# Performance work log

Hardware: AMD Instinct MI355X
Metric: run time of the kernel (lower is better)

## Reference

```python
import jax, jax.numpy as jnp
import numpy as np

B, S, D, H = 2, 2048, 1024, 16
DH = D // H  # dim per head (dim_singl_head)
SCALE = 0.02


def layer_norm(x, g, b, eps=1e-5):
    m = jnp.mean(x, axis=-1, keepdims=True)
    v = jnp.mean((x - m) ** 2, axis=-1, keepdims=True)
    return (x - m) / jnp.sqrt(v + eps) * g + b


def setup_inputs() -> dict:
    key = jax.random.key(0)
    ks = jax.random.split(key, 12)
    return {
        "query": jax.random.normal(ks[0], (B, S, D), jnp.float32),
        "key": jax.random.normal(ks[1], (B, S, D), jnp.float32),
        "value": jax.random.normal(ks[2], (B, S, D), jnp.float32),
        "mask": jax.random.randint(ks[3], (B, S), 0, 2).astype(jnp.int32),
        "Wq": jax.random.normal(ks[4], (D, D), jnp.float32) * SCALE,
        "bq": jnp.zeros((D,), jnp.float32),
        "Wk": jax.random.normal(ks[5], (D, D), jnp.float32) * SCALE,
        "bk": jnp.zeros((D,), jnp.float32),
        "Wv": jax.random.normal(ks[6], (D, D), jnp.float32) * SCALE,
        "bv": jnp.zeros((D,), jnp.float32),
        "g_att": jnp.ones((DH,), jnp.float32),
        "b_att": jnp.zeros((DH,), jnp.float32),
        "Wres": jax.random.normal(ks[7], (D, D), jnp.float32) * SCALE,
        "bres": jnp.zeros((D,), jnp.float32),
        "g_out": jnp.ones((D,), jnp.float32),
        "b_out": jnp.zeros((D,), jnp.float32),
    }


def reference(query, key, value, mask, Wq, bq, Wk, bk, Wv, bv,
              g_att, b_att, Wres, bres, g_out, b_out):
    # split heads: torch's split(dh,-1)+cat(dim=0) == [H,B,S,dh] layout
    def heads(x):
        return x.reshape(B, S, H, DH).transpose(2, 0, 1, 3)  # [H,B,S,dh]

    q = heads(query @ Wq + bq)
    k = heads(key @ Wk + bk)
    v = heads(value @ Wv + bv)

    # additive mask: (1-mask)*-1e9, broadcast [1,B,1,Sk]
    madd = (1.0 - mask.astype(q.dtype))[None, :, None, :] * -1e9

    scores = jnp.einsum('hbqd,hbkd->hbqk', q, k) / np.float32(np.sqrt(DH))
    w = jax.nn.softmax(scores + madd, axis=-1)
    out = jnp.einsum('hbqk,hbkd->hbqd', w, v)

    out = out + q                         # residual_att
    out = layer_norm(out, g_att, b_att)   # per-head LayerNorm on dh

    # concat heads back: [H,B,S,dh] -> [B,S,H*dh]
    out = out.transpose(1, 2, 0, 3).reshape(B, S, D)

    out = out + jnp.tanh(out @ Wres + bres)  # residual_out branch
    out = layer_norm(out, g_out, b_out)      # norm_out
    return jnp.tanh(out)                     # final activation
```

## Files before the change

### kernel.cpp

```cpp
#include <hip/hip_runtime.h>
#include <cstdint>
#include <cstddef>

#define BB 2
#define SS 2048
#define DD 1024
#define HH 16
#define DHH 64
#define MROWS (BB*SS)

typedef short short8 __attribute__((ext_vector_type(8)));
typedef short short4v __attribute__((ext_vector_type(4)));
typedef float floatx4 __attribute__((ext_vector_type(4)));
typedef float floatx16 __attribute__((ext_vector_type(16)));
typedef unsigned int uint4v __attribute__((ext_vector_type(4)));

#define GAS __attribute__((address_space(1)))
#define LAS __attribute__((address_space(3)))

__device__ __forceinline__ float4 ld4(const float* p) { return *(const float4*)p; }

__device__ __forceinline__ short f2bf(float x) {
    unsigned u = __builtin_bit_cast(unsigned, x);
    unsigned r = (u + 0x7fffu + ((u >> 16) & 1u)) >> 16;
    return (short)r;
}

__device__ __forceinline__ unsigned cvtpk(float lo, float hi) {
    unsigned r;
    asm("v_cvt_pk_bf16_f32 %0, %1, %2" : "=v"(r) : "v"(lo), "v"(hi));
    return r;
}

__device__ __forceinline__ void gl_lds16(const short* g, short* l) {
    __builtin_amdgcn_global_load_lds((const GAS unsigned int*)g,
                                     (LAS unsigned int*)l, 16, 0, 0);
}

__global__ __launch_bounds__(256) void convert_kernel(
    const float* __restrict__ s0, const float* __restrict__ s1, const float* __restrict__ s2,
    short* __restrict__ d0, short* __restrict__ d1, short* __restrict__ d2)
{
    const float* s; short* d;
    if (blockIdx.z == 0)      { s = s0; d = d0; }
    else if (blockIdx.z == 1) { s = s1; d = d1; }
    else                      { s = s2; d = d2; }
    size_t idx = ((size_t)blockIdx.x * 256 + threadIdx.x) * 8;
    float4 a = ld4(s + idx);
    float4 b = ld4(s + idx + 4);
    short8 p;
    p[0] = f2bf(a.x); p[1] = f2bf(a.y); p[2] = f2bf(a.z); p[3] = f2bf(a.w);
    p[4] = f2bf(b.x); p[5] = f2bf(b.y); p[6] = f2bf(b.z); p[7] = f2bf(b.w);
    *(short8*)(d + idx) = p;
}

__global__ __launch_bounds__(256) void transpose_w_kernel(
    const float* __restrict__ W0, const float* __restrict__ W1,
    const float* __restrict__ W2, const float* __restrict__ W3,
    short* __restrict__ T0, short* __restrict__ T1,
    short* __restrict__ T2, short* __restrict__ T3)
{
    const float* W; short* T;
    if (blockIdx.z == 0)      { W = W0; T = T0; }
    else if (blockIdx.z == 1) { W = W1; T = T1; }
    else if (blockIdx.z == 2) { W = W2; T = T2; }
    else                      { W = W3; T = T3; }

    __shared__ short tile[64 * 72];
    const int t  = threadIdx.x;
    const int k0 = blockIdx.x * 64, n0 = blockIdx.y * 64;
#pragma unroll
    for (int i = 0; i < 4; i++) {
        int flat = i * 256 + t;
        int row = flat >> 4;
        int c4  = (flat & 15) * 4;
        float4 v = ld4(W + (size_t)(k0 + row) * DD + n0 + c4);
        tile[(c4 + 0) * 72 + row] = f2bf(v.x);
        tile[(c4 + 1) * 72 + row] = f2bf(v.y);
        tile[(c4 + 2) * 72 + row] = f2bf(v.z);
        tile[(c4 + 3) * 72 + row] = f2bf(v.w);
    }
    __syncthreads();
#pragma unroll
    for (int i = 0; i < 4; i++) {
        int flat = i * 256 + t;
        int nrow = flat >> 4;
        int kc   = (flat & 15) * 4;
        short4v pk = *(short4v*)&tile[nrow * 72 + kc];
        *(short4v*)(T + (size_t)(n0 + nrow) * DD + k0 + kc) = pk;
    }
}

__global__ __launch_bounds__(256) void gemm_bf16_kernel(
    const short* __restrict__ A0, const short* __restrict__ A1, const short* __restrict__ A2,
    const short* __restrict__ Bt0, const short* __restrict__ Bt1, const short* __restrict__ Bt2,
    const float* __restrict__ b0, const float* __restrict__ b1, const float* __restrict__ b2,
    float* __restrict__ Cf0, float* __restrict__ Cf1, float* __restrict__ Cf2,
    short* __restrict__ Cb0, short* __restrict__ Cb1, short* __restrict__ Cb2,
    short* __restrict__ Ct0, short* __restrict__ Ct1, short* __restrict__ Ct2,
    float cs0, float cs1, float cs2)
{
    const short* A; const short* Bt; const float* bias;
    float* Cf; short* Cb; short* Ct; float cbs;
    if (blockIdx.z == 0)      { A = A0; Bt = Bt0; bias = b0; Cf = Cf0; Cb = Cb0; Ct = Ct0; cbs = cs0; }
    else if (blockIdx.z == 1) { A = A1; Bt = Bt1; bias = b1; Cf = Cf1; Cb = Cb1; Ct = Ct1; cbs = cs1; }
    else                      { A = A2; Bt = Bt2; bias = b2; Cf = Cf2; Cb = Cb2; Ct = Ct2; cbs = cs2; }

    __shared__ __align__(16) short As[128 * 32];
    __shared__ __align__(16) short Bs[128 * 32];

    const int tid  = threadIdx.x;
    const int lane = tid & 63;
    const int wave = tid >> 6;
    const int quad = lane >> 4;
    const int l15  = lane & 15;
    const int m0 = blockIdx.y * 128;
    const int n0 = blockIdx.x * 128;
    const int wr = (wave >> 1) * 64;
    const int wc = (wave & 1) * 64;

    floatx4 acc[4][4];
#pragma unroll
    for (int mt = 0; mt < 4; mt++)
#pragma unroll
        for (int nt = 0; nt < 4; nt++) acc[mt][nt] = (floatx4)0.0f;

    for (int k0 = 0; k0 < DD; k0 += 32) {
        __syncthreads();
#pragma unroll
        for (int j = 0; j < 2; j++) {
            int chunk = j * 256 + tid;
            int row = chunk >> 2;
            int ch  = chunk & 3;
            gl_lds16(A  + (size_t)(m0 + row) * DD + k0 + ch * 8, &As[chunk * 8]);
            gl_lds16(Bt + (size_t)(n0 + row) * DD + k0 + ch * 8, &Bs[chunk * 8]);
        }
        __syncthreads();

        short8 af[4], bf[4];
#pragma unroll
        for (int mt = 0; mt < 4; mt++)
            af[mt] = *(const short8*)&As[(wr + mt * 16 + l15) * 32 + quad * 8];
#pragma unroll
        for (int nt = 0; nt < 4; nt++)
            bf[nt] = *(const short8*)&Bs[(wc + nt * 16 + l15) * 32 + quad * 8];
#pragma unroll
        for (int mt = 0; mt < 4; mt++)
#pragma unroll
            for (int nt = 0; nt < 4; nt++)
                acc[mt][nt] = __builtin_amdgcn_mfma_f32_16x16x32_bf16(af[mt], bf[nt], acc[mt][nt], 0, 0, 0);
    }

    float biasv[4];
#pragma unroll
    for (int nt = 0; nt < 4; nt++) biasv[nt] = bias[n0 + wc + nt * 16 + l15];

    if (Cf || Cb) {
#pragma unroll
        for (int mt = 0; mt < 4; mt++)
#pragma unroll
            for (int r = 0; r < 4; r++) {
                const int m = m0 + wr + mt * 16 + quad * 4 + r;
                const size_t rowb = (size_t)m * DD + n0 + wc;
#pragma unroll
                for (int nt = 0; nt < 4; nt++) {
                    float v = acc[mt][nt][r] + biasv[nt];
                    if (Cf) Cf[rowb + nt * 16 + l15] = v;
                    if (Cb) Cb[rowb + nt * 16 + l15] = f2bf(v * cbs);
                }
            }
    }
    if (Ct) {
#pragma unroll
        for (int mt = 0; mt < 4; mt++) {
            const int mbase = m0 + wr + mt * 16 + quad * 4;
            const int bb = mbase >> 11;
            const int s0 = mbase & 2047;
#pragma unroll
            for (int nt = 0; nt < 4; nt++) {
                const int c = n0 + wc + nt * 16 + l15;
                short4v pk;
#pragma unroll
                for (int r = 0; r < 4; r++) pk[r] = f2bf(acc[mt][nt][r] + biasv[nt]);
                *(short4v*)(Ct + ((size_t)(bb * 1024 + c)) * SS + s0) = pk;
            }
        }
    }
}

__global__ __launch_bounds__(256) void repack_kernel(
    const short* __restrict__ Kb, const short* __restrict__ Vt,
    const int* __restrict__ mask,
    short* __restrict__ Kf, short* __restrict__ Vf, float* __restrict__ maddf)
{
    const int t = threadIdx.x;
    if (blockIdx.z == 0) {
        const int b = blockIdx.x >> 6, kg = blockIdx.x & 63;
#pragma unroll
        for (int i = 0; i < 16; i++) {
            const int h = i, ks = t >> 6, lane = t & 63;
            const int c = lane & 31, hi = lane >> 5;
            short8 v = *(const short8*)(Kb + (size_t)(b * 2048 + kg * 32 + c) * 1024
                                        + h * 64 + ks * 16 + hi * 8);
            *(short8*)(Kf + ((size_t)((b * 16 + h) * 64 + kg)) * 2048 + ks * 512 + lane * 8) = v;
        }
    } else if (blockIdx.x < 64) {
        const int b = blockIdx.x >> 5, kt = blockIdx.x & 31;
#pragma unroll
        for (int i = 0; i < 32; i++) {
            const int flat = i * 256 + t;
            const int h = flat >> 9, rest = flat & 511;
            const int tp = rest >> 7, dg = (rest >> 6) & 1, lane = rest & 63;
            const int c = lane & 31, hi = lane >> 5;
            short8 v = *(const short8*)(Vt + (size_t)(b * 1024 + h * 64 + dg * 32 + c) * 2048
                                        + kt * 64 + tp * 16 + hi * 8);
            *(short8*)(Vf + ((size_t)((b * 16 + h) * 32 + kt)) * 4096
                       + (tp * 2 + dg) * 512 + lane * 8) = v;
        }
    } else if (blockIdx.x < 66) {
        const int b = blockIdx.x - 64;
#pragma unroll
        for (int j = 0; j < 8; j++) {
            const int idx = t * 8 + j;
            maddf[b * 2048 + idx] = (1.0f - (float)mask[b * 2048 + idx]) * -1e9f;
        }
    }
}

__device__ __forceinline__ void attn_tile(
    const short8 (&kf)[2][4], const short8 (&vf)[8], const short8 (&qf)[4],
    const float* mdb, int kt, floatx16 (&o)[2], float& lsum)
{
#pragma unroll
    for (int g = 0; g < 2; g++) {
        floatx16 acc = (floatx16)0.0f;
        __builtin_amdgcn_s_setprio(1);
#pragma unroll
        for (int ks = 0; ks < 4; ks++)
            acc = __builtin_amdgcn_mfma_f32_32x32x16_bf16(kf[g][ks], qf[ks], acc, 0, 0, 0);
        __builtin_amdgcn_s_setprio(0);
        float p[16];
#pragma unroll
        for (int a = 0; a < 4; a++) {
            float4 mr = *(const float4*)(mdb + kt * 64 + g * 32 + a * 8);
            p[4 * a + 0] = __builtin_exp2f(acc[4 * a + 0] + mr.x);
            p[4 * a + 1] = __builtin_exp2f(acc[4 * a + 1] + mr.y);
            p[4 * a + 2] = __builtin_exp2f(acc[4 * a + 2] + mr.z);
            p[4 * a + 3] = __builtin_exp2f(acc[4 * a + 3] + mr.w);
        }
        lsum += ((p[0] + p[1]) + (p[2] + p[3])) + ((p[4] + p[5]) + (p[6] + p[7]))
              + ((p[8] + p[9]) + (p[10] + p[11])) + ((p[12] + p[13]) + (p[14] + p[15]));
#pragma unroll
        for (int t2 = 0; t2 < 2; t2++) {
            unsigned w0 = cvtpk(p[8 * t2 + 0], p[8 * t2 + 1]);
            unsigned w1 = cvtpk(p[8 * t2 + 2], p[8 * t2 + 3]);
            unsigned w2 = cvtpk(p[8 * t2 + 4], p[8 * t2 + 5]);
            unsigned w3 = cvtpk(p[8 * t2 + 6], p[8 * t2 + 7]);
            asm volatile("v_permlane32_swap_b32 %0, %1" : "+v"(w0), "+v"(w2));
            asm volatile("v_permlane32_swap_b32 %0, %1" : "+v"(w1), "+v"(w3));
            uint4v u = {w0, w1, w2, w3};
            short8 pa = __builtin_bit_cast(short8, u);
            __builtin_amdgcn_s_setprio(1);
#pragma unroll
            for (int dg = 0; dg < 2; dg++)
                o[dg] = __builtin_amdgcn_mfma_f32_32x32x16_bf16(
                    pa, vf[(g * 2 + t2) * 2 + dg], o[dg], 0, 0, 0);
            __builtin_amdgcn_s_setprio(0);
        }
    }
}

__global__ __launch_bounds__(256, 2) void attn_mfma_kernel(
    const short* __restrict__ Qb, const short* __restrict__ Kf, const short* __restrict__ Vf,
    const float* __restrict__ Qf, const float* __restrict__ maddf,
    const float* __restrict__ g_att, const float* __restrict__ b_att,
    float* __restrict__ X, short* __restrict__ Xb)
{
    const int tid  = threadIdx.x;
    const int lane = tid & 63;
    const int wave = tid >> 6;
    const int hi   = lane >> 5;
    const int c    = lane & 31;

    const int h  = blockIdx.y;
    const int b  = blockIdx.z;
    const int q0 = blockIdx.x * 128;
    const int bS = b * SS;

    const short* kfb = Kf + ((size_t)(b * 16 + h) * 64) * 2048 + lane * 8;
    const short* vfb = Vf + ((size_t)(b * 16 + h) * 32) * 4096 + lane * 8;
    const float* mdb = maddf + b * 2048 + hi * 4;

    short8 qf[4];
#pragma unroll
    for (int ks = 0; ks < 4; ks++)
        qf[ks] = *(const short8*)(Qb +
            (size_t)(bS + q0 + wave * 32 + c) * DD + h * 64 + ks * 16 + hi * 8);

    floatx16 o[2];
    o[0] = (floatx16)0.0f;
    o[1] = (floatx16)0.0f;
    float lsum = 0.0f;

    short8 kfA[2][4], kfB[2][4], vf[8];
#pragma unroll
    for (int g = 0; g < 2; g++)
#pragma unroll
        for (int ks = 0; ks < 4; ks++)
            kfA[g][ks] = *(const short8*)(kfb + (size_t)(0 * 2 + g) * 2048 + ks * 512);

    for (int kt = 0; kt < 32; kt += 2) {
#pragma unroll
        for (int j = 0; j < 8; j++)
            vf[j] = *(const short8*)(vfb + (size_t)kt * 4096 + j * 512);
#pragma unroll
        for (int g = 0; g < 2; g++)
#pragma unroll
            for (int ks = 0; ks < 4; ks++)
                kfB[g][ks] = *(const short8*)(kfb + (size_t)((kt + 1) * 2 + g) * 2048 + ks * 512);
        attn_tile(kfA, vf, qf, mdb, kt, o, lsum);

#pragma unroll
        for (int j = 0; j < 8; j++)
            vf[j] = *(const short8*)(vfb + (size_t)(kt + 1) * 4096 + j * 512);
        const int ktn = (kt + 2 < 32) ? (kt + 2) : 31;
#pragma unroll
        for (int g = 0; g < 2; g++)
#pragma unroll
            for (int ks = 0; ks < 4; ks++)
                kfA[g][ks] = *(const short8*)(kfb + (size_t)(ktn * 2 + g) * 2048 + ks * 512);
        attn_tile(kfB, vf, qf, mdb, kt + 1, o, lsum);
    }

    lsum += __shfl_xor(lsum, 32);
    const float rl = 1.0f / lsum;

    const float g0v = g_att[c], g1v = g_att[32 + c];
    const float b0v = b_att[c], b1v = b_att[32 + c];

#pragma unroll
    for (int r = 0; r < 16; r++) {
        const int rloc = (r & 3) + 8 * (r >> 2) + 4 * hi;
        const float rlr = __shfl(rl, rloc);
        const int row = q0 + wave * 32 + rloc;
        const size_t base = (size_t)(bS + row) * DD + h * 64;
        float x0 = o[0][r] * rlr + Qf[base + c];
        float x1 = o[1][r] * rlr + Qf[base + 32 + c];
        float s = x0 + x1;
#pragma unroll
        for (int off = 1; off < 32; off <<= 1) s += __shfl_xor(s, off);
        const float mu = s * (1.0f / 64.0f);
        float d0 = x0 - mu, d1 = x1 - mu;
        float v = d0 * d0 + d1 * d1;
#pragma unroll
        for (int off = 1; off < 32; off <<= 1) v += __shfl_xor(v, off);
        const float rstd = rsqrtf(v * (1.0f / 64.0f) + 1e-5f);
        float y0 = d0 * rstd * g0v + b0v;
        float y1 = d1 * rstd * g1v + b1v;
        X[base + c]      = y0;
        X[base + 32 + c] = y1;
        Xb[base + c]      = f2bf(y0);
        Xb[base + 32 + c] = f2bf(y1);
    }
}

__global__ __launch_bounds__(256) void lnout_kernel(
    const float* __restrict__ X, const float* __restrict__ Y,
    const float* __restrict__ g, const float* __restrict__ bcoef,
    float* __restrict__ out)
{
    const int r = blockIdx.x;
    const int t = threadIdx.x;
    const size_t base = (size_t)r * DD + (t << 2);
    float4 x = ld4(X + base);
    float4 y = ld4(Y + base);
    float4 z;
    z.x = x.x + tanhf(y.x);
    z.y = x.y + tanhf(y.y);
    z.z = x.z + tanhf(y.z);
    z.w = x.w + tanhf(y.w);

    __shared__ float red[4];
    __shared__ float stats[2];
    const int w = t >> 6;

    float sv = z.x + z.y + z.z + z.w;
#pragma unroll
    for (int off = 32; off > 0; off >>= 1) sv += __shfl_down(sv, off);
    if ((t & 63) == 0) red[w] = sv;
    __syncthreads();
    if (t == 0) stats[0] = (red[0] + red[1] + red[2] + red[3]) * (1.0f / 1024.0f);
    __syncthreads();
    const float mu = stats[0];

    float4 d;
    d.x = z.x - mu; d.y = z.y - mu; d.z = z.z - mu; d.w = z.w - mu;
    float s2 = d.x * d.x + d.y * d.y + d.z * d.z + d.w * d.w;
#pragma unroll
    for (int off = 32; off > 0; off >>= 1) s2 += __shfl_down(s2, off);
    if ((t & 63) == 0) red[w] = s2;
    __syncthreads();
    if (t == 0) stats[1] = rsqrtf((red[0] + red[1] + red[2] + red[3]) * (1.0f / 1024.0f) + 1e-5f);
    __syncthreads();
    const float rstd = stats[1];

    float4 gv = ld4(g + (t << 2));
    float4 bv = ld4(bcoef + (t << 2));
    float4 o;
    o.x = tanhf(d.x * rstd * gv.x + bv.x);
    o.y = tanhf(d.y * rstd * gv.y + bv.y);
    o.z = tanhf(d.z * rstd * gv.z + bv.z);
    o.w = tanhf(d.w * rstd * gv.w + bv.w);
    *(float4*)(out + base) = o;
}

extern "C" void kernel_launch(void* const* d_in, const int* in_sizes, int n_in,
                              void* d_out, int out_size, void* d_ws, size_t ws_size,
                              hipStream_t stream)
{
    const float* query = (const float*)d_in[0];
    const float* key   = (const float*)d_in[1];
    const float* value = (const float*)d_in[2];
    const int*   mask  = (const int*)  d_in[3];
    const float* Wq    = (const float*)d_in[4];
    const float* bq    = (const float*)d_in[5];
    const float* Wk    = (const float*)d_in[6];
    const float* bk    = (const float*)d_in[7];
    const float* Wv    = (const float*)d_in[8];
    const float* bv    = (const float*)d_in[9];
    const float* g_att = (const float*)d_in[10];
    const float* b_att = (const float*)d_in[11];
    const float* Wres  = (const float*)d_in[12];
    const float* bres  = (const float*)d_in[13];
    const float* g_out = (const float*)d_in[14];
    const float* b_out = (const float*)d_in[15];

    const size_t MAT = (size_t)MROWS * DD;
    float* fws = (float*)d_ws;
    float* Qw = fws;
    float* Xw = fws + MAT;
    short* Qb = (short*)(fws + 2 * MAT);
    short* Kb = Qb + MAT;
    short* Vt = Kb + MAT;
    short* qbf = Vt + MAT;
    short* kbf = qbf + MAT;
    short* vbf = kbf + MAT;
    short* Wtq = vbf + MAT;
    short* Wtk = Wtq + DD * DD;
    short* Wtv = Wtk + DD * DD;
    short* Wtr = Wtv + DD * DD;
    float* maddf = (float*)(Wtr + DD * DD);
    short* Xb = qbf;
    short* Kf = vbf;
    short* Vf = kbf;
    float* Yw = (float*)kbf;

    convert_kernel<<<dim3(MAT / 2048, 1, 3), 256, 0, stream>>>(
        query, key, value, qbf, kbf, vbf);

    transpose_w_kernel<<<dim3(16, 16, 4), 256, 0, stream>>>(
        Wq, Wk, Wv, Wres, Wtq, Wtk, Wtv, Wtr);

    gemm_bf16_kernel<<<dim3(8, 32, 3), 256, 0, stream>>>(
        qbf, kbf, vbf, Wtq, Wtk, Wtv, bq, bk, bv,
        Qw, nullptr, nullptr,
        Qb, Kb, nullptr,
        nullptr, nullptr, Vt,
        0.180336884f, 1.0f, 1.0f);

    repack_kernel<<<dim3(128, 1, 2), 256, 0, stream>>>(
        Kb, Vt, mask, Kf, Vf, maddf);

    attn_mfma_kernel<<<dim3(SS / 128, HH, BB), 256, 0, stream>>>(
        Qb, Kf, Vf, Qw, maddf, g_att, b_att, Xw, Xb);

    gemm_bf16_kernel<<<dim3(8, 32, 1), 256, 0, stream>>>(
        Xb, Xb, Xb, Wtr, Wtr, Wtr, bres, bres, bres,
        Yw, Yw, Yw, nullptr, nullptr, nullptr, nullptr, nullptr, nullptr,
        1.0f, 1.0f, 1.0f);

    lnout_kernel<<<MROWS, 256, 0, stream>>>(Xw, Yw, g_out, b_out, (float*)d_out);
}
```

Baseline: 305.9 us.

## Split attention key range across wave pairs and split-K the output GEMM

```diff
diff --git a/kernel.cpp b/kernel.cpp
--- a/kernel.cpp
+++ b/kernel.cpp
@@ -98,7 +98,7 @@
     float* __restrict__ Cf0, float* __restrict__ Cf1, float* __restrict__ Cf2,
     short* __restrict__ Cb0, short* __restrict__ Cb1, short* __restrict__ Cb2,
     short* __restrict__ Ct0, short* __restrict__ Ct1, short* __restrict__ Ct2,
-    float cs0, float cs1, float cs2)
+    float cs0, float cs1, float cs2, int ksplit)
 {
     const short* A; const short* Bt; const float* bias;
     float* Cf; short* Cb; short* Ct; float cbs;
@@ -119,13 +119,16 @@
     const int wr = (wave >> 1) * 64;
     const int wc = (wave & 1) * 64;
 
+    const int kbeg = ksplit ? (int)blockIdx.z * 512 : 0;
+    const int kend = ksplit ? kbeg + 512 : DD;
+
     floatx4 acc[4][4];
 #pragma unroll
     for (int mt = 0; mt < 4; mt++)
 #pragma unroll
         for (int nt = 0; nt < 4; nt++) acc[mt][nt] = (floatx4)0.0f;
 
-    for (int k0 = 0; k0 < DD; k0 += 32) {
+    for (int k0 = kbeg; k0 < kend; k0 += 32) {
         __syncthreads();
 #pragma unroll
         for (int j = 0; j < 2; j++) {
@@ -270,7 +273,7 @@
     }
 }
 
-__global__ __launch_bounds__(256, 2) void attn_mfma_kernel(
+__global__ __launch_bounds__(512, 4) void attn_mfma_kernel(
     const short* __restrict__ Qb, const short* __restrict__ Kf, const short* __restrict__ Vf,
     const float* __restrict__ Qf, const float* __restrict__ maddf,
     const float* __restrict__ g_att, const float* __restrict__ b_att,
@@ -279,6 +282,8 @@
     const int tid  = threadIdx.x;
     const int lane = tid & 63;
     const int wave = tid >> 6;
+    const int qsub = wave >> 1;
+    const int kh   = wave & 1;
     const int hi   = lane >> 5;
     const int c    = lane & 31;
 
@@ -287,6 +292,9 @@
     const int q0 = blockIdx.x * 128;
     const int bS = b * SS;
 
+    __shared__ float olds[4][32][64];
+    __shared__ float lsums[4][64];
+
     const short* kfb = Kf + ((size_t)(b * 16 + h) * 64) * 2048 + lane * 8;
     const short* vfb = Vf + ((size_t)(b * 16 + h) * 32) * 4096 + lane * 8;
     const float* mdb = maddf + b * 2048 + hi * 4;
@@ -295,21 +303,22 @@
 #pragma unroll
     for (int ks = 0; ks < 4; ks++)
         qf[ks] = *(const short8*)(Qb +
-            (size_t)(bS + q0 + wave * 32 + c) * DD + h * 64 + ks * 16 + hi * 8);
+            (size_t)(bS + q0 + qsub * 32 + c) * DD + h * 64 + ks * 16 + hi * 8);
 
     floatx16 o[2];
     o[0] = (floatx16)0.0f;
     o[1] = (floatx16)0.0f;
     float lsum = 0.0f;
 
+    const int kbase = kh * 16;
     short8 kfA[2][4], kfB[2][4], vf[8];
 #pragma unroll
     for (int g = 0; g < 2; g++)
 #pragma unroll
         for (int ks = 0; ks < 4; ks++)
-            kfA[g][ks] = *(const short8*)(kfb + (size_t)(0 * 2 + g) * 2048 + ks * 512);
-
-    for (int kt = 0; kt < 32; kt += 2) {
+            kfA[g][ks] = *(const short8*)(kfb + (size_t)(kbase * 2 + g) * 2048 + ks * 512);
+
+    for (int kt = kbase; kt < kbase + 16; kt += 2) {
 #pragma unroll
         for (int j = 0; j < 8; j++)
             vf[j] = *(const short8*)(vfb + (size_t)kt * 4096 + j * 512);
@@ -323,7 +332,7 @@
 #pragma unroll
         for (int j = 0; j < 8; j++)
             vf[j] = *(const short8*)(vfb + (size_t)(kt + 1) * 4096 + j * 512);
-        const int ktn = (kt + 2 < 32) ? (kt + 2) : 31;
+        const int ktn = (kt + 2 < kbase + 16) ? (kt + 2) : (kbase + 15);
 #pragma unroll
         for (int g = 0; g < 2; g++)
 #pragma unroll
@@ -332,6 +341,23 @@
         attn_tile(kfB, vf, qf, mdb, kt + 1, o, lsum);
     }
 
+    if (kh == 1) {
+#pragma unroll
+        for (int r = 0; r < 16; r++) {
+            olds[qsub][r][lane]      = o[0][r];
+            olds[qsub][16 + r][lane] = o[1][r];
+        }
+        lsums[qsub][lane] = lsum;
+    }
+    __syncthreads();
+    if (kh == 1) return;
+#pragma unroll
+    for (int r = 0; r < 16; r++) {
+        o[0][r] += olds[qsub][r][lane];
+        o[1][r] += olds[qsub][16 + r][lane];
+    }
+    lsum += lsums[qsub][lane];
+
     lsum += __shfl_xor(lsum, 32);
     const float rl = 1.0f / lsum;
 
@@ -342,7 +368,7 @@
     for (int r = 0; r < 16; r++) {
         const int rloc = (r & 3) + 8 * (r >> 2) + 4 * hi;
         const float rlr = __shfl(rl, rloc);
-        const int row = q0 + wave * 32 + rloc;
+        const int row = q0 + qsub * 32 + rloc;
         const size_t base = (size_t)(bS + row) * DD + h * 64;
         float x0 = o[0][r] * rlr + Qf[base + c];
         float x1 = o[1][r] * rlr + Qf[base + 32 + c];
@@ -365,20 +391,23 @@
 }
 
 __global__ __launch_bounds__(256) void lnout_kernel(
-    const float* __restrict__ X, const float* __restrict__ Y,
+    const float* __restrict__ X, const float* __restrict__ Y1,
+    const float* __restrict__ Y2, const float* __restrict__ bres,
     const float* __restrict__ g, const float* __restrict__ bcoef,
     float* __restrict__ out)
 {
     const int r = blockIdx.x;
     const int t = threadIdx.x;
     const size_t base = (size_t)r * DD + (t << 2);
-    float4 x = ld4(X + base);
-    float4 y = ld4(Y + base);
+    float4 x  = ld4(X + base);
+    float4 y1 = ld4(Y1 + base);
+    float4 y2 = ld4(Y2 + base);
+    float4 br = ld4(bres + (t << 2));
     float4 z;
-    z.x = x.x + tanhf(y.x);
-    z.y = x.y + tanhf(y.y);
-    z.z = x.z + tanhf(y.z);
-    z.w = x.w + tanhf(y.w);
+    z.x = x.x + tanhf(y1.x + y2.x - br.x);
+    z.y = x.y + tanhf(y1.y + y2.y - br.y);
+    z.z = x.z + tanhf(y1.z + y2.z - br.z);
+    z.w = x.w + tanhf(y1.w + y2.w - br.w);
 
     __shared__ float red[4];
     __shared__ float stats[2];
@@ -453,7 +482,8 @@
     short* Xb = qbf;
     short* Kf = vbf;
     short* Vf = kbf;
-    float* Yw = (float*)kbf;
+    float* Y1 = (float*)kbf;
+    float* Y2 = Qw;
 
     convert_kernel<<<dim3(MAT / 2048, 1, 3), 256, 0, stream>>>(
         query, key, value, qbf, kbf, vbf);
@@ -466,18 +496,18 @@
         Qw, nullptr, nullptr,
         Qb, Kb, nullptr,
         nullptr, nullptr, Vt,
-        0.180336884f, 1.0f, 1.0f);
+        0.180336884f, 1.0f, 1.0f, 0);
 
     repack_kernel<<<dim3(128, 1, 2), 256, 0, stream>>>(
         Kb, Vt, mask, Kf, Vf, maddf);
 
-    attn_mfma_kernel<<<dim3(SS / 128, HH, BB), 256, 0, stream>>>(
+    attn_mfma_kernel<<<dim3(SS / 128, HH, BB), 512, 0, stream>>>(
         Qb, Kf, Vf, Qw, maddf, g_att, b_att, Xw, Xb);
 
-    gemm_bf16_kernel<<<dim3(8, 32, 1), 256, 0, stream>>>(
+    gemm_bf16_kernel<<<dim3(8, 32, 2), 256, 0, stream>>>(
         Xb, Xb, Xb, Wtr, Wtr, Wtr, bres, bres, bres,
-        Yw, Yw, Yw, nullptr, nullptr, nullptr, nullptr, nullptr, nullptr,
-        1.0f, 1.0f, 1.0f);
-
-    lnout_kernel<<<MROWS, 256, 0, stream>>>(Xw, Yw, g_out, b_out, (float*)d_out);
-}
+        Y1, Y2, nullptr, nullptr, nullptr, nullptr, nullptr, nullptr, nullptr,
+        1.0f, 1.0f, 1.0f, 1);
+
+    lnout_kernel<<<MROWS, 256, 0, stream>>>(Xw, Y1, Y2, bres, g_out, b_out, (float*)d_out);
+}
```

Result: slower. 542.4 us (+77.3%).
